# Kernel tuning notes

Hardware: AMD Instinct MI355X
Metric: run time of the kernel (lower is better)

Reference implementation:

```python
import jax, jax.numpy as jnp
import numpy as np

SCALE = 15.0
BIG = 1e9  # masked-out distances; exp(-SCALE*BIG) underflows to exactly 0 in fp32
P, M, N, D, NCAM = 6, 512, 4096, 1024, 8
FEAT_STD = 0.03  # keep squared distances O(1) so exp(-scale*d) doesn't underflow


def setup_inputs() -> dict:
    key = jax.random.key(0)
    k1, k2, k3, k4 = jax.random.split(key, 4)
    feature = jax.random.normal(k1, (P, M, D), dtype=jnp.float32) * FEAT_STD
    centers = jax.random.normal(k2, (P, N, D), dtype=jnp.float32) * FEAT_STD
    camid = jax.random.randint(k3, (M,), 0, NCAM)   # camera id per sample
    cam = jax.random.randint(k4, (N,), 0, NCAM)     # camera id per center
    return {"feature": feature, "camid": camid, "centers": centers, "cam": cam}


def _explog(x):
    # faithful to torch: (-scale * x).exp().sum().log(), per row (last axis)
    return jnp.log(jnp.sum(jnp.exp(-SCALE * x), axis=-1))


def reference(feature, camid, centers, cam):
    p, m, d = feature.shape
    n = centers.shape[1]
    # squared euclidean distance map per part: [P, m, n]
    f2 = jnp.sum(feature * feature, axis=-1)            # [P, m]
    c2 = jnp.sum(centers * centers, axis=-1)            # [P, n]
    dist = f2[:, :, None] + c2[:, None, :] - 2.0 * jnp.einsum('pmd,pnd->pmn', feature, centers)
    # intra mask: center cam == sample cam  (same for all parts)
    mask = camid[:, None] == cam[None, :]               # [m, n]
    # push masked-out entries to BIG so ascending sort puts them last and exp(-s*BIG)=0
    d_intra = jnp.sort(jnp.where(mask[None, :, :], dist, BIG), axis=-1)   # [P, m, n]
    d_inter = jnp.sort(jnp.where(mask[None, :, :], BIG, dist), axis=-1)   # [P, m, n]
    x_intra = _explog(d_intra[..., :4])
    y_intra = _explog(d_intra[..., 6:])
    x_inter = _explog(d_inter[..., :8])
    y_inter = _explog(d_inter[..., 12:])
    hinge_intra = jnp.maximum(-x_intra + y_intra + 12.0, 0.0)
    hinge_inter = jnp.maximum(-x_inter + y_inter + 5.0, 0.0)
    loss = jnp.sum(hinge_intra + hinge_inter) / (m * p)
    return loss
```

## Files before the change

kernel.cpp:

```cpp
#include <hip/hip_runtime.h>
#include <math.h>

#define PP 6
#define MM 512
#define NN 4096
#define DD 1024
#define KSCALE 15.0f
#define BIGV 1e9f

#define BM 128
#define BN 128
#define BK 16
#define NCHUNK (DD / BK)
#define NSTRIP (NN / BN)
#define KI 6
#define KR 12
#define PARTW 20
#define LDSB 16384
#define NBUF 4

typedef __bf16 bf16x8 __attribute__((ext_vector_type(8)));
typedef float  f32x16 __attribute__((ext_vector_type(16)));

__device__ __forceinline__ void insert6(float (&a)[KI], float v) {
    if (v < a[KI - 1]) {
        float cur = v;
#pragma unroll
        for (int x = 0; x < KI; ++x) {
            float lo = fminf(a[x], cur);
            float hi = fmaxf(a[x], cur);
            a[x] = lo; cur = hi;
        }
    }
}
__device__ __forceinline__ void insert12(float (&a)[KR], float v) {
    if (v < a[KR - 1]) {
        float cur = v;
#pragma unroll
        for (int x = 0; x < KR; ++x) {
            float lo = fminf(a[x], cur);
            float hi = fmaxf(a[x], cur);
            a[x] = lo; cur = hi;
        }
    }
}


__global__ __launch_bounds__(256)
void decomp_all(const float* __restrict__ feature, const float* __restrict__ centers,
                __bf16* __restrict__ Fhi, __bf16* __restrict__ Flo,
                __bf16* __restrict__ Chi, __bf16* __restrict__ Clo,
                float* __restrict__ c2, float* __restrict__ out) {
    if (blockIdx.x == 0 && threadIdx.x == 0) out[0] = 0.0f;
    const int r    = blockIdx.x * 4 + (threadIdx.x >> 6);
    const int lane = threadIdx.x & 63;
    const float* src;
    __bf16 *dhi, *dlo;
    int row;
    bool isC;
    if (r < PP * MM) { src = feature; dhi = Fhi; dlo = Flo; row = r; isC = false; }
    else             { src = centers; dhi = Chi; dlo = Clo; row = r - PP * MM; isC = true; }
    const size_t eb = (size_t)row * DD + lane * 16;
    float s = 0.0f;
#pragma unroll
    for (int g = 0; g < 2; ++g) {
        float4 v0 = *(const float4*)(src + eb + g * 8);
        float4 v1 = *(const float4*)(src + eb + g * 8 + 4);
        float fv[8] = {v0.x, v0.y, v0.z, v0.w, v1.x, v1.y, v1.z, v1.w};
        bf16x8 h, l;
#pragma unroll
        for (int i = 0; i < 8; ++i) {
            s = fmaf(fv[i], fv[i], s);
            __bf16 hh = (__bf16)fv[i];
            h[i] = hh;
            l[i] = (__bf16)(fv[i] - (float)hh);
        }
        *(bf16x8*)(dhi + eb + g * 8) = h;
        *(bf16x8*)(dlo + eb + g * 8) = l;
    }
#pragma unroll
    for (int off = 32; off > 0; off >>= 1) s += __shfl_down(s, off, 64);
    if (isC && lane == 0) c2[row] = s;
}


__global__ __launch_bounds__(256, 2)
void dist_topk_kernel(const __bf16* __restrict__ Fhi, const __bf16* __restrict__ Flo,
                      const __bf16* __restrict__ Chi, const __bf16* __restrict__ Clo,
                      const float* __restrict__ c2g,
                      const int* __restrict__ camid, const int* __restrict__ cam,
                      float* __restrict__ partials) {
    const int ns = blockIdx.x;
    const int mt = blockIdx.y;
    const int p  = blockIdx.z;
    const int t  = threadIdx.x;
    const int lane = t & 63, w = t >> 6;
    const int wr = w >> 1, wc = w & 1;
    const int l31 = lane & 31, lh = lane >> 5;

    __shared__ __align__(16) char smem[NBUF * LDSB];
    __shared__ int s_cam[BN];
    float* bandS = (float*)smem;

    const char* srcp[4];
    int ldsoff[4];
#pragma unroll
    for (int i = 0; i < 4; ++i) {
        const int r_idx = w * 4 + i;
        const int plane = r_idx >> 3;
        const int ks    = (r_idx >> 2) & 1;
        const int row   = (r_idx & 3) * 64 + lane;
        const __bf16* basep;
        size_t gr;
        if (row < BM) { basep = plane ? Flo : Fhi; gr = (size_t)(p * MM + mt * BM + row) * DD; }
        else          { basep = plane ? Clo : Chi; gr = (size_t)(p * NN + ns * BN + row - BM) * DD; }
        srcp[i]   = (const char*)(basep + gr + ks * 8);
        ldsoff[i] = r_idx * 1024;
    }

    int aU[2], bU[2];
#pragma unroll
    for (int x = 0; x < 2; ++x) {
        aU[x] = (lh * 256 + wr * 64 + x * 32 + l31) * 16;
        bU[x] = (lh * 256 + 128 + wc * 64 + x * 32 + l31) * 16;
    }

    f32x16 acc[2][2];
#pragma unroll
    for (int i = 0; i < 2; ++i)
#pragma unroll
        for (int j = 0; j < 2; ++j)
#pragma unroll
            for (int r = 0; r < 16; ++r) acc[i][j][r] = 0.0f;

    auto stage = [&](int buf, int c) {
#pragma unroll
        for (int i = 0; i < 4; ++i)
            __builtin_amdgcn_global_load_lds(
                (const __attribute__((address_space(1))) void*)(srcp[i] + (size_t)c * 32),
                (__attribute__((address_space(3))) void*)(smem + buf * LDSB + ldsoff[i]),
                16, 0, 0);
    };

    stage(0, 0); stage(1, 1); stage(2, 2);

    for (int c = 0; c < NCHUNK; ++c) {
        if (c + 2 < NCHUNK)      asm volatile("s_waitcnt vmcnt(8)" ::: "memory");
        else if (c + 1 < NCHUNK) asm volatile("s_waitcnt vmcnt(4)" ::: "memory");
        else                     asm volatile("s_waitcnt vmcnt(0)" ::: "memory");
        __builtin_amdgcn_s_barrier();
        if (c + 3 < NCHUNK) stage((c + 3) & 3, c + 3);

        const char* bb = smem + (c & 3) * LDSB;
        bf16x8 ah[2], al[2], bh[2], bl[2];
#pragma unroll
        for (int x = 0; x < 2; ++x) {
            ah[x] = *(const bf16x8*)(bb + aU[x]);
            al[x] = *(const bf16x8*)(bb + 8192 + aU[x]);
            bh[x] = *(const bf16x8*)(bb + bU[x]);
            bl[x] = *(const bf16x8*)(bb + 8192 + bU[x]);
        }
        asm volatile("s_waitcnt lgkmcnt(0)" ::: "memory");
        __builtin_amdgcn_sched_barrier(0);
        __builtin_amdgcn_s_setprio(1);
#pragma unroll
        for (int mi = 0; mi < 2; ++mi)
#pragma unroll
            for (int nj = 0; nj < 2; ++nj) {
                acc[mi][nj] = __builtin_amdgcn_mfma_f32_32x32x16_bf16(
                    ah[mi], bh[nj], acc[mi][nj], 0, 0, 0);
                acc[mi][nj] = __builtin_amdgcn_mfma_f32_32x32x16_bf16(
                    ah[mi], bl[nj], acc[mi][nj], 0, 0, 0);
                acc[mi][nj] = __builtin_amdgcn_mfma_f32_32x32x16_bf16(
                    al[mi], bh[nj], acc[mi][nj], 0, 0, 0);
            }
        __builtin_amdgcn_s_setprio(0);
    }

    __syncthreads();

    if (t < BN) s_cam[t] = cam[ns * BN + t];
    float c2v[2];
#pragma unroll
    for (int nj = 0; nj < 2; ++nj)
        c2v[nj] = c2g[p * NN + ns * BN + wc * 64 + nj * 32 + l31];

    const int myrow = t >> 1, half = t & 1;
    const int my_cam = camid[mt * BM + myrow];
    float ti[KI], tr[KR];
#pragma unroll
    for (int x = 0; x < KI; ++x) ti[x] = BIGV;
#pragma unroll
    for (int x = 0; x < KR; ++x) tr[x] = BIGV;
    float si = 0.0f, sr = 0.0f;

#pragma unroll
    for (int b = 0; b < 4; ++b) {
        __syncthreads();
        if (wc == (b >> 1)) {
            const int nj = b & 1;
#pragma unroll
            for (int mi = 0; mi < 2; ++mi)
#pragma unroll
                for (int r = 0; r < 16; ++r) {
                    int R = wr * 64 + mi * 32 + (r & 3) + 8 * (r >> 2) + 4 * lh;
                    bandS[R * 33 + l31] = c2v[nj] - 2.0f * acc[mi][nj][r];
                }
        }
        __syncthreads();
        const float* drow = bandS + myrow * 33 + half * 16;
        const int*   crow = s_cam + b * 32 + half * 16;
#pragma unroll
        for (int j = 0; j < 16; ++j) {
            float dd = drow[j];
            float e  = __expf(-KSCALE * dd);
            if (crow[j] == my_cam) { si += e; insert6(ti, dd); }
            else                   { sr += e; insert12(tr, dd); }
        }
    }

    float oti[KI], otr[KR];
#pragma unroll
    for (int x = 0; x < KI; ++x) oti[x] = __shfl_xor(ti[x], 1, 64);
#pragma unroll
    for (int x = 0; x < KR; ++x) otr[x] = __shfl_xor(tr[x], 1, 64);
    float osi = __shfl_xor(si, 1, 64), osr = __shfl_xor(sr, 1, 64);
#pragma unroll
    for (int x = 0; x < KI; ++x) insert6(ti, oti[x]);
#pragma unroll
    for (int x = 0; x < KR; ++x) insert12(tr, otr[x]);
    si += osi; sr += osr;

    if (!half) {
        float* outp = partials +
            ((size_t)(p * MM + mt * BM + myrow) * NSTRIP + ns) * PARTW;
#pragma unroll
        for (int x = 0; x < KI; ++x) outp[x] = ti[x];
#pragma unroll
        for (int x = 0; x < KR; ++x) outp[KI + x] = tr[x];
        outp[18] = si; outp[19] = sr;
    }
}


__global__ __launch_bounds__(256)
void finalize_kernel(const float* __restrict__ partials, float* __restrict__ out) {
    const int t = threadIdx.x, lane = t & 63, w = t >> 6;
    const int row = blockIdx.x * 4 + w;
    const int strip = lane & 31;
    const float* q = partials + ((size_t)row * NSTRIP + strip) * PARTW;
    float ti[KI], tr[KR];
#pragma unroll
    for (int x = 0; x < KI; ++x) ti[x] = q[x];
#pragma unroll
    for (int x = 0; x < KR; ++x) tr[x] = q[KI + x];
    float si = q[18], sr = q[19];

#pragma unroll
    for (int s = 1; s < 32; s <<= 1) {
        float oti[KI], otr[KR];
#pragma unroll
        for (int x = 0; x < KI; ++x) oti[x] = __shfl_xor(ti[x], s, 64);
#pragma unroll
        for (int x = 0; x < KR; ++x) otr[x] = __shfl_xor(tr[x], s, 64);
        float osi = __shfl_xor(si, s, 64), osr = __shfl_xor(sr, s, 64);
#pragma unroll
        for (int x = 0; x < KI; ++x) insert6(ti, oti[x]);
#pragma unroll
        for (int x = 0; x < KR; ++x) insert12(tr, otr[x]);
        si += osi; sr += osr;
    }

    if (lane == 0) {
        float ei[KI], er[KR];
#pragma unroll
        for (int x = 0; x < KI; ++x) ei[x] = __expf(-KSCALE * ti[x]);
#pragma unroll
        for (int x = 0; x < KR; ++x) er[x] = __expf(-KSCALE * tr[x]);
        float x_intra = logf(ei[0] + ei[1] + ei[2] + ei[3]);
        float top6 = ei[0] + ei[1] + ei[2] + ei[3] + ei[4] + ei[5];
        float y_intra = logf(fmaxf(si - top6, 0.0f));
        float x_inter = logf(er[0] + er[1] + er[2] + er[3] +
                             er[4] + er[5] + er[6] + er[7]);
        float top12 = 0.0f;
#pragma unroll
        for (int x = 0; x < KR; ++x) top12 += er[x];
        float y_inter = logf(fmaxf(sr - top12, 0.0f));
        float h = fmaxf(y_intra - x_intra + 12.0f, 0.0f) +
                  fmaxf(y_inter - x_inter + 5.0f, 0.0f);
        atomicAdd(out, h * (1.0f / (MM * PP)));
    }
}

extern "C" void kernel_launch(void* const* d_in, const int* in_sizes, int n_in,
                              void* d_out, int out_size, void* d_ws, size_t ws_size,
                              hipStream_t stream) {
    const float* feature = (const float*)d_in[0];
    const int*   camid   = (const int*)  d_in[1];
    const float* centers = (const float*)d_in[2];
    const int*   cam     = (const int*)  d_in[3];
    float* out = (float*)d_out;

    char* ws = (char*)d_ws;
    __bf16* Chi = (__bf16*)(ws);
    __bf16* Clo = (__bf16*)(ws + 50331648);
    __bf16* Fhi = (__bf16*)(ws + 100663296);
    __bf16* Flo = (__bf16*)(ws + 106954752);
    float*  c2  = (float*) (ws + 113246208);
    float*  partials = (float*)(ws + 113344512);

    decomp_all<<<(PP * (MM + NN)) / 4, 256, 0, stream>>>(feature, centers,
                                                         Fhi, Flo, Chi, Clo,
                                                         c2, out);
    dim3 grid(NSTRIP, MM / BM, PP);
    dist_topk_kernel<<<grid, 256, 0, stream>>>(Fhi, Flo, Chi, Clo, c2,
                                               camid, cam, partials);
    finalize_kernel<<<(PP * MM) / 4, 256, 0, stream>>>(partials, out);
}
```

Measured before the change: 385.4 us.

## Fuse centers bf16 split and norm into distance kernel, stage via registers

The separate pass that splits the centers tensor into hi/lo bf16 planes and computes their squared norms is removed. The distance kernel now loads fp32 centers straight into registers, converts them, accumulates c2 and writes the bf16 planes into LDS, while feature tiles still use direct global-to-LDS loads. The pipeline drops to triple buffering and occupancy is raised to 3 blocks per CU. This avoids writing and re-reading roughly 100 MB of bf16 center planes, but each center chunk is now re-read as fp32 and converted once per M-tile, and the register staging adds VALU work and latency to the main loop.

```diff
diff --git a/kernel.cpp b/kernel.cpp
--- a/kernel.cpp
+++ b/kernel.cpp
@@ -17,7 +17,7 @@
 #define KR 12
 #define PARTW 20
 #define LDSB 16384
-#define NBUF 4
+#define NBUF 3
 
 typedef __bf16 bf16x8 __attribute__((ext_vector_type(8)));
 typedef float  f32x16 __attribute__((ext_vector_type(16)));
@@ -45,49 +45,49 @@
     }
 }
 
+__device__ __forceinline__ void cvt8(const float4& v0, const float4& v1,
+                                     bf16x8& hi, bf16x8& lo) {
+    float f[8] = {v0.x, v0.y, v0.z, v0.w, v1.x, v1.y, v1.z, v1.w};
+#pragma unroll
+    for (int i = 0; i < 8; ++i) {
+        __bf16 h = (__bf16)f[i];
+        hi[i] = h;
+        lo[i] = (__bf16)(f[i] - (float)h);
+    }
+}
+
+__device__ __forceinline__ float sq8(const float4& a, const float4& b) {
+    float s = a.x * a.x;
+    s = fmaf(a.y, a.y, s); s = fmaf(a.z, a.z, s); s = fmaf(a.w, a.w, s);
+    s = fmaf(b.x, b.x, s); s = fmaf(b.y, b.y, s);
+    s = fmaf(b.z, b.z, s); s = fmaf(b.w, b.w, s);
+    return s;
+}
+
 
 __global__ __launch_bounds__(256)
-void decomp_all(const float* __restrict__ feature, const float* __restrict__ centers,
-                __bf16* __restrict__ Fhi, __bf16* __restrict__ Flo,
-                __bf16* __restrict__ Chi, __bf16* __restrict__ Clo,
-                float* __restrict__ c2, float* __restrict__ out) {
+void decomp_feat(const float* __restrict__ f,
+                 __bf16* __restrict__ Fhi, __bf16* __restrict__ Flo,
+                 float* __restrict__ out) {
     if (blockIdx.x == 0 && threadIdx.x == 0) out[0] = 0.0f;
-    const int r    = blockIdx.x * 4 + (threadIdx.x >> 6);
+    const int row  = blockIdx.x * 4 + (threadIdx.x >> 6);
     const int lane = threadIdx.x & 63;
-    const float* src;
-    __bf16 *dhi, *dlo;
-    int row;
-    bool isC;
-    if (r < PP * MM) { src = feature; dhi = Fhi; dlo = Flo; row = r; isC = false; }
-    else             { src = centers; dhi = Chi; dlo = Clo; row = r - PP * MM; isC = true; }
-    const size_t eb = (size_t)row * DD + lane * 16;
-    float s = 0.0f;
 #pragma unroll
     for (int g = 0; g < 2; ++g) {
-        float4 v0 = *(const float4*)(src + eb + g * 8);
-        float4 v1 = *(const float4*)(src + eb + g * 8 + 4);
-        float fv[8] = {v0.x, v0.y, v0.z, v0.w, v1.x, v1.y, v1.z, v1.w};
+        const size_t eb = (size_t)row * DD + g * 512 + lane * 8;
+        float4 v0 = *(const float4*)(f + eb);
+        float4 v1 = *(const float4*)(f + eb + 4);
         bf16x8 h, l;
-#pragma unroll
-        for (int i = 0; i < 8; ++i) {
-            s = fmaf(fv[i], fv[i], s);
-            __bf16 hh = (__bf16)fv[i];
-            h[i] = hh;
-            l[i] = (__bf16)(fv[i] - (float)hh);
-        }
-        *(bf16x8*)(dhi + eb + g * 8) = h;
-        *(bf16x8*)(dlo + eb + g * 8) = l;
-    }
-#pragma unroll
-    for (int off = 32; off > 0; off >>= 1) s += __shfl_down(s, off, 64);
-    if (isC && lane == 0) c2[row] = s;
-}
-
-
-__global__ __launch_bounds__(256, 2)
+        cvt8(v0, v1, h, l);
+        *(bf16x8*)(Fhi + eb) = h;
+        *(bf16x8*)(Flo + eb) = l;
+    }
+}
+
+
+__global__ __launch_bounds__(256, 3)
 void dist_topk_kernel(const __bf16* __restrict__ Fhi, const __bf16* __restrict__ Flo,
-                      const __bf16* __restrict__ Chi, const __bf16* __restrict__ Clo,
-                      const float* __restrict__ c2g,
+                      const float* __restrict__ centers,
                       const int* __restrict__ camid, const int* __restrict__ cam,
                       float* __restrict__ partials) {
     const int ns = blockIdx.x;
@@ -99,30 +99,30 @@
     const int l31 = lane & 31, lh = lane >> 5;
 
     __shared__ __align__(16) char smem[NBUF * LDSB];
-    __shared__ int s_cam[BN];
+    __shared__ int   s_cam[BN];
+    __shared__ float c2buf[BM][2];
     float* bandS = (float*)smem;
 
-    const char* srcp[4];
-    int ldsoff[4];
-#pragma unroll
-    for (int i = 0; i < 4; ++i) {
-        const int r_idx = w * 4 + i;
-        const int plane = r_idx >> 3;
-        const int ks    = (r_idx >> 2) & 1;
-        const int row   = (r_idx & 3) * 64 + lane;
-        const __bf16* basep;
-        size_t gr;
-        if (row < BM) { basep = plane ? Flo : Fhi; gr = (size_t)(p * MM + mt * BM + row) * DD; }
-        else          { basep = plane ? Clo : Chi; gr = (size_t)(p * NN + ns * BN + row - BM) * DD; }
-        srcp[i]   = (const char*)(basep + gr + ks * 8);
-        ldsoff[i] = r_idx * 1024;
-    }
+    const char* asrc[2];
+    int aldso[2];
+#pragma unroll
+    for (int i = 0; i < 2; ++i) {
+        const int rme = t + i * 256;
+        const __bf16* basep = ((rme >> 8) & 1) ? Flo : Fhi;
+        asrc[i] = (const char*)(basep +
+                  (size_t)(p * MM + mt * BM + (rme & 127)) * DD + ((rme >> 7) & 1) * 8);
+        const int rb = w * 64 + i * 256;
+        aldso[i] = ((rb >> 8) & 1) * 4096 + ((rb >> 7) & 1) * 2048 + (rb & 127) * 16;
+    }
+    const int brow = t & 127, bo = t >> 7;
+    const float* bsrc = centers + (size_t)(p * NN + ns * BN + brow) * DD + bo * 8;
+    const int bwo = bo * 2048 + brow * 16;
 
     int aU[2], bU[2];
 #pragma unroll
     for (int x = 0; x < 2; ++x) {
-        aU[x] = (lh * 256 + wr * 64 + x * 32 + l31) * 16;
-        bU[x] = (lh * 256 + 128 + wc * 64 + x * 32 + l31) * 16;
+        aU[x] = lh * 2048 + (wr * 64 + x * 32 + l31) * 16;
+        bU[x] = 8192 + lh * 2048 + (wc * 64 + x * 32 + l31) * 16;
     }
 
     f32x16 acc[2][2];
@@ -133,32 +133,45 @@
 #pragma unroll
             for (int r = 0; r < 16; ++r) acc[i][j][r] = 0.0f;
 
-    auto stage = [&](int buf, int c) {
-#pragma unroll
-        for (int i = 0; i < 4; ++i)
+    float c2acc = 0.0f;
+
+    auto issueA = [&](int c) {
+        char* dst = smem + (c % 3) * LDSB;
+#pragma unroll
+        for (int i = 0; i < 2; ++i)
             __builtin_amdgcn_global_load_lds(
-                (const __attribute__((address_space(1))) void*)(srcp[i] + (size_t)c * 32),
-                (__attribute__((address_space(3))) void*)(smem + buf * LDSB + ldsoff[i]),
+                (const __attribute__((address_space(1))) void*)(asrc[i] + (size_t)c * 32),
+                (__attribute__((address_space(3))) void*)(dst + aldso[i]),
                 16, 0, 0);
     };
-
-    stage(0, 0); stage(1, 1); stage(2, 2);
-
-    for (int c = 0; c < NCHUNK; ++c) {
-        if (c + 2 < NCHUNK)      asm volatile("s_waitcnt vmcnt(8)" ::: "memory");
-        else if (c + 1 < NCHUNK) asm volatile("s_waitcnt vmcnt(4)" ::: "memory");
-        else                     asm volatile("s_waitcnt vmcnt(0)" ::: "memory");
+    auto issueB = [&](int c, float4& b0, float4& b1) {
+        const float4* src = (const float4*)(bsrc + (size_t)c * 16);
+        b0 = src[0]; b1 = src[1];
+    };
+    auto step = [&](int c, float4& b0, float4& b1) {
+        if (c + 1 < NCHUNK) asm volatile("s_waitcnt vmcnt(4)" ::: "memory");
+        else                asm volatile("s_waitcnt vmcnt(0)" ::: "memory");
+        {
+            bf16x8 h, l;
+            cvt8(b0, b1, h, l);
+            c2acc += sq8(b0, b1);
+            char* dst = smem + (c % 3) * LDSB;
+            *(bf16x8*)(dst + 8192  + bwo) = h;
+            *(bf16x8*)(dst + 12288 + bwo) = l;
+        }
+        asm volatile("s_waitcnt lgkmcnt(0)" ::: "memory");
         __builtin_amdgcn_s_barrier();
-        if (c + 3 < NCHUNK) stage((c + 3) & 3, c + 3);
-
-        const char* bb = smem + (c & 3) * LDSB;
+        __builtin_amdgcn_sched_barrier(0);
+        if (c + 2 < NCHUNK) { issueA(c + 2); issueB(c + 2, b0, b1); }
+
+        const char* bb = smem + (c % 3) * LDSB;
         bf16x8 ah[2], al[2], bh[2], bl[2];
 #pragma unroll
         for (int x = 0; x < 2; ++x) {
             ah[x] = *(const bf16x8*)(bb + aU[x]);
-            al[x] = *(const bf16x8*)(bb + 8192 + aU[x]);
+            al[x] = *(const bf16x8*)(bb + 4096 + aU[x]);
             bh[x] = *(const bf16x8*)(bb + bU[x]);
-            bl[x] = *(const bf16x8*)(bb + 8192 + bU[x]);
+            bl[x] = *(const bf16x8*)(bb + 4096 + bU[x]);
         }
         asm volatile("s_waitcnt lgkmcnt(0)" ::: "memory");
         __builtin_amdgcn_sched_barrier(0);
@@ -175,15 +188,29 @@
                     al[mi], bh[nj], acc[mi][nj], 0, 0, 0);
             }
         __builtin_amdgcn_s_setprio(0);
+    };
+
+    float4 be0, be1, bo0, bo1;
+    issueA(0); issueB(0, be0, be1);
+    issueA(1); issueB(1, bo0, bo1);
+
+    for (int c = 0; c < NCHUNK; c += 2) {
+        step(c,     be0, be1);
+        step(c + 1, bo0, bo1);
     }
 
     __syncthreads();
 
+    c2buf[brow][bo] = c2acc;
     if (t < BN) s_cam[t] = cam[ns * BN + t];
+    __syncthreads();
+
     float c2v[2];
 #pragma unroll
-    for (int nj = 0; nj < 2; ++nj)
-        c2v[nj] = c2g[p * NN + ns * BN + wc * 64 + nj * 32 + l31];
+    for (int nj = 0; nj < 2; ++nj) {
+        const int C = wc * 64 + nj * 32 + l31;
+        c2v[nj] = c2buf[C][0] + c2buf[C][1];
+    }
 
     const int myrow = t >> 1, half = t & 1;
     const int my_cam = camid[mt * BM + myrow];
@@ -302,18 +329,13 @@
     float* out = (float*)d_out;
 
     char* ws = (char*)d_ws;
-    __bf16* Chi = (__bf16*)(ws);
-    __bf16* Clo = (__bf16*)(ws + 50331648);
-    __bf16* Fhi = (__bf16*)(ws + 100663296);
-    __bf16* Flo = (__bf16*)(ws + 106954752);
-    float*  c2  = (float*) (ws + 113246208);
-    float*  partials = (float*)(ws + 113344512);
-
-    decomp_all<<<(PP * (MM + NN)) / 4, 256, 0, stream>>>(feature, centers,
-                                                         Fhi, Flo, Chi, Clo,
-                                                         c2, out);
+    __bf16* Fhi = (__bf16*)(ws);
+    __bf16* Flo = (__bf16*)(ws + 6291456);
+    float*  partials = (float*)(ws + 12582912);
+
+    decomp_feat<<<(PP * MM) / 4, 256, 0, stream>>>(feature, Fhi, Flo, out);
     dim3 grid(NSTRIP, MM / BM, PP);
-    dist_topk_kernel<<<grid, 256, 0, stream>>>(Fhi, Flo, Chi, Clo, c2,
+    dist_topk_kernel<<<grid, 256, 0, stream>>>(Fhi, Flo, centers,
                                                camid, cam, partials);
     finalize_kernel<<<(PP * MM) / 4, 256, 0, stream>>>(partials, out);
 }
```

New measurement: 337.1 us. 12.5% less time.
